# Kernel optimization log

Measured on AMD Instinct MI355X. Metric: run time of the kernel, lower is better.

The kernel has to match this reference:

```python
import jax, jax.numpy as jnp
import numpy as np

RATE = 2
KSIZE = 3          # patch size for similarity
KERNEL = 2 * RATE  # patch size for alpha scatter (4)
BN_EPS = 1e-5


def _extract_patches(x, k, s):
    """Mirror of GuidedCxtAtten.extract_patches: reflect-pad then unfold.
    x: [B,C,H,W] -> [B,Ho,Wo,C,k,k] with Ho=H//s, Wo=W//s."""
    left = (k - s + 1) // 2
    right = (k - s) // 2
    xp = jnp.pad(x, ((0, 0), (0, 0), (left, right), (left, right)), mode='reflect')
    Hp, Wp = xp.shape[2], xp.shape[3]
    Ho = (Hp - k) // s + 1
    Wo = (Wp - k) // s + 1
    ii = (jnp.arange(Ho) * s)[:, None] + jnp.arange(k)[None, :]   # [Ho,k]
    jj = (jnp.arange(Wo) * s)[:, None] + jnp.arange(k)[None, :]   # [Wo,k]
    p = xp[:, :, ii[:, :, None, None], jj[None, None, :, :]]      # [B,C,Ho,k,Wo,k]
    return p.transpose(0, 2, 4, 1, 3, 5)                          # [B,Ho,Wo,C,k,k]


def setup_inputs() -> dict:
    key = jax.random.key(0)
    ks = jax.random.split(key, 5)
    B, Cg, Ca, H, W = 4, 256, 128, 128, 128
    f = jax.random.normal(ks[0], (B, Cg, H, W), dtype=jnp.float32)
    alpha = jax.random.normal(ks[1], (B, Ca, H, W), dtype=jnp.float32)
    unknown = (jax.random.uniform(ks[2], (B, 1, H, W)) > 0.5).astype(jnp.float32)
    # guidance_conv: 1x1, Cg -> Cg//2, xavier-ish
    gc_w = jax.random.normal(ks[3], (Cg // 2, Cg), dtype=jnp.float32) * np.sqrt(2.0 / (Cg + Cg // 2))
    gc_b = jnp.zeros((Cg // 2,), dtype=jnp.float32)
    # W[0]: 1x1 conv Ca->Ca no bias; W[1]: BN with gamma=0.001, beta=0 per init
    w_w = jax.random.normal(ks[4], (Ca, Ca), dtype=jnp.float32) * np.sqrt(1.0 / Ca)
    bn_gamma = jnp.full((Ca,), 0.001, dtype=jnp.float32)
    bn_beta = jnp.zeros((Ca,), dtype=jnp.float32)
    return {"f": f, "alpha": alpha, "unknown": unknown, "gc_w": gc_w, "gc_b": gc_b,
            "w_w": w_w, "bn_gamma": bn_gamma, "bn_beta": bn_beta}


def _forward(f, alpha, unknown, gc_w, gc_b, w_w, bn_gamma, bn_beta):
    # guidance 1x1 conv
    fg = jnp.einsum('oi,bihw->bohw', gc_w, f) + gc_b[None, :, None, None]
    B, _, H, W = fg.shape
    Ca = alpha.shape[1]
    Hs, Ws = H // RATE, W // RATE
    L = Hs * Ws

    # alpha patches [B,L,Ca,4,4] (kernel=2*rate, stride=rate)
    alpha_w = _extract_patches(alpha, KERNEL, RATE).reshape(B, L, Ca, KERNEL, KERNEL)

    # nearest downsample by rate (torch nearest with scale 1/2 == strided pick)
    f_ds = fg[:, :, ::RATE, ::RATE]                # [B,Cg/2,Hs,Ws]
    unk_ds = unknown[:, :, ::RATE, ::RATE]         # [B,1,Hs,Ws]

    # similarity filter patches [B,L,C,3,3]
    w = _extract_patches(f_ds, KSIZE, 1).reshape(B, L, -1, KSIZE, KSIZE)

    # known/unknown softmax scales [B,2]
    u_mean = unk_ds.mean(axis=(2, 3))              # [B,1]
    k_mean = 1.0 - u_mean
    su = jnp.clip(jnp.sqrt(u_mean / k_mean), 0.1, 10.0)
    sk = jnp.clip(jnp.sqrt(k_mean / u_mean), 0.1, 10.0)
    softmax_scale = jnp.concatenate([su, sk], axis=1)

    # patch-mean of unknown mask -> binary patch mask [B,L]
    m = _extract_patches(unk_ds, KSIZE, 1).reshape(B, L, -1).mean(axis=2)
    mm = (m > 0.0).astype(fg.dtype)

    # l2-normalize filters per patch, then correlate against all positions.
    # Conv of reflect-padded f_ds with stride-1 3x3 patch filters == inner
    # product of normalized patches with the raw patches (same extraction).
    norm = jnp.sqrt(jnp.sum(w * w, axis=(2, 3, 4), keepdims=True))
    w_normed = w / jnp.maximum(norm, 1e-4)
    scores = jnp.einsum('bqcij,bpcij->bqp', w_normed, w)   # [B,L(q=patch),L(p=pos)]

    # known/unknown scaling per source patch q
    gate = jnp.where(mm > 0.0, su, sk)                      # [B,L]
    scores = scores * gate[:, :, None]

    # self-match suppression only for unknown patches (diagonal q == p)
    diag = jnp.arange(L)
    scores = scores.at[:, diag, diag].add(-10000.0 * mm)

    attn = jax.nn.softmax(scores, axis=1)                   # softmax over patches q

    # offsets (argmax patch per position, relative to center)
    idx = jnp.argmax(attn, axis=1)                          # [B,L]
    offsets = jnp.stack([idx // Ws, idx % Ws], axis=1).reshape(B, 2, Hs, Ws)
    offsets = offsets - jnp.array([Hs // 2, Ws // 2]).reshape(1, 2, 1, 1)

    # scatter alpha patches with attention weights: per-sample conv_transpose2d
    attn_map = attn.reshape(B, L, Hs, Ws)

    def ct(yi, wc):  # yi [L,Hs,Ws], wc [L,Ca,4,4]
        rhs = jnp.flip(wc, (2, 3)).transpose(1, 0, 2, 3)    # [Ca,L,4,4]
        pad = KERNEL - 1 - 1                                # torch padding=1
        out = jax.lax.conv_general_dilated(
            yi[None], rhs, window_strides=(1, 1),
            padding=[(pad, pad), (pad, pad)], lhs_dilation=(RATE, RATE),
            dimension_numbers=('NCHW', 'OIHW', 'NCHW'))
        return out[0]

    y = jax.vmap(ct)(attn_map, alpha_w) / 4.0               # [B,Ca,H,W]

    # W: 1x1 conv (no bias) + BatchNorm2d (training-mode batch stats)
    yw = jnp.einsum('oi,bihw->bohw', w_w, y)
    mean = yw.mean(axis=(0, 2, 3))
    var = yw.var(axis=(0, 2, 3))
    yn = (yw - mean[None, :, None, None]) * jax.lax.rsqrt(var + BN_EPS)[None, :, None, None]
    yn = yn * bn_gamma[None, :, None, None] + bn_beta[None, :, None, None]

    return yn + alpha, offsets, softmax_scale


def reference(f, alpha, unknown, gc_w, gc_b, w_w, bn_gamma, bn_beta):
    return _forward(f, alpha, unknown, gc_w, gc_b, w_w, bn_gamma, bn_beta)
```

## Files before the change

kernel.cpp:

```cpp
#include <hip/hip_runtime.h>
#include <math.h>

#define B 4
#define CG 256
#define CM 128
#define CA 128
#define H 128
#define W_ 128
#define HS 64
#define WS 64
#define L 4096
#define D1 1152
#define D2 2048
#define NPIX 65536
#define NT2 128

#define STP_F 8388608UL
#define WF_F  4718592UL
#define ZB_F  4194304UL
#define SLOT_F (STP_F + WF_F + ZB_F)

typedef unsigned short u16;
typedef __attribute__((ext_vector_type(8))) short short8v;
typedef __attribute__((ext_vector_type(4))) unsigned short u16x4;
typedef __attribute__((ext_vector_type(4))) float f32x4;

__device__ __forceinline__ float bf2f(u16 x) {
    union { unsigned int u; float f; } v; v.u = ((unsigned int)x) << 16; return v.f;
}
__device__ __forceinline__ u16 f2bf(float x) {
    union { float f; unsigned int u; } v; v.f = x;
    unsigned int r = (v.u + 0x7FFFu + ((v.u >> 16) & 1u)) >> 16;
    return (u16)r;
}
__device__ __forceinline__ void gll16(const void* g, void* l) {
    __builtin_amdgcn_global_load_lds((const __attribute__((address_space(1))) void*)g,
                                     (__attribute__((address_space(3))) void*)l, 16, 0, 0);
}
__device__ __forceinline__ int refl(int i, int n) {
    return i < 0 ? -i : (i >= n ? 2 * n - 2 - i : i);
}
__device__ __forceinline__ int swz(int row, int fq) {
    return row * 32 + ((fq ^ ((row >> 1) & 3)) * 8);
}

__device__ __forceinline__ void stage32(const u16* __restrict__ mat, int rowTile,
                                        int kt, u16* lds, int wid, int lane) {
#pragma unroll
    for (int c = 0; c < 2; ++c) {
        int off = c * 8192 + wid * 1024 + lane * 16;
        int row = off >> 6;
        int cb  = off & 63;
        const u16* g = mat + (size_t)(rowTile + row) * L + kt * 32
                     + ((cb ^ (((row >> 1) & 3) << 4)) >> 1);
        gll16(g, (char*)lds + c * 8192 + wid * 1024);
    }
}
__device__ __forceinline__ short8v rdfrag32(const u16* lds, int r, int fq) {
    return *(const short8v*)((const char*)lds + r * 64 + ((fq * 16) ^ (((r >> 1) & 3) << 4)));
}

__global__ __launch_bounds__(256) void k_conv_ds(const float* __restrict__ f,
                                                 const float* __restrict__ gw,
                                                 const float* __restrict__ gb,
                                                 float* __restrict__ fds,
                                                 float* __restrict__ ssq) {
    __shared__ float sf[CG * 64];
    __shared__ float part[4][64];
    int t = threadIdx.x;
    int hs = blockIdx.x, b = blockIdx.y;
    const float* fb = f + (size_t)b * CG * H * W_ + (2 * hs) * W_;
    for (int idx = t; idx < CG * 64; idx += 256) {
        int ci = idx >> 6, ws = idx & 63;
        sf[idx] = fb[(size_t)ci * H * W_ + 2 * ws];
    }
    __syncthreads();
    int ws = t & 63;
    int wave = __builtin_amdgcn_readfirstlane(t >> 6);
    const float* gwp = gw + (size_t)(wave * 32) * CG;
    float acc[32];
#pragma unroll
    for (int r = 0; r < 32; ++r) acc[r] = gb[wave * 32 + r];
    for (int ci = 0; ci < CG; ++ci) {
        float fv = sf[ci * 64 + ws];
#pragma unroll
        for (int r = 0; r < 32; ++r) acc[r] += gwp[r * CG + ci] * fv;
    }
    float sq = 0.f;
#pragma unroll
    for (int r = 0; r < 32; ++r) {
        int co = wave * 32 + r;
        fds[(((size_t)b * CM + co) * HS + hs) * WS + ws] = acc[r];
        sq += acc[r] * acc[r];
    }
    part[wave][ws] = sq;
    __syncthreads();
    if (t < 64)
        ssq[((size_t)b * HS + hs) * WS + t] =
            part[0][t] + part[1][t] + part[2][t] + part[3][t];
}

__global__ __launch_bounds__(256) void k_scale(const float* __restrict__ unk,
                                               float* __restrict__ suk,
                                               float* __restrict__ out2) {
    int b = blockIdx.x, t = threadIdx.x;
    __shared__ float red[256];
    float s = 0.f;
    for (int i = t; i < L; i += 256) {
        int hs = i >> 6, ws = i & 63;
        s += unk[(size_t)b * H * W_ + (2 * hs) * W_ + 2 * ws];
    }
    red[t] = s;
    __syncthreads();
    for (int o = 128; o > 0; o >>= 1) {
        if (t < o) red[t] += red[t + o];
        __syncthreads();
    }
    if (t == 0) {
        float u = red[0] / (float)L;
        float k = 1.0f - u;
        float su = sqrtf(u / k); su = fminf(fmaxf(su, 0.1f), 10.0f);
        float sk = sqrtf(k / u); sk = fminf(fmaxf(sk, 0.1f), 10.0f);
        suk[b * 2] = su; suk[b * 2 + 1] = sk;
        out2[b * 2] = su; out2[b * 2 + 1] = sk;
    }
}

__global__ __launch_bounds__(64) void k_gate(const float* __restrict__ unk,
                                             const float* __restrict__ ssq,
                                             const float* __restrict__ suk,
                                             float* __restrict__ g,
                                             float* __restrict__ dg) {
    int ws = threadIdx.x, hs = blockIdx.x, b = blockIdx.y;
    float sm = 0.f, sq = 0.f;
    for (int di = -1; di <= 1; ++di) {
        int rh = refl(hs + di, HS);
        for (int dj = -1; dj <= 1; ++dj) {
            int rw = refl(ws + dj, WS);
            sm += unk[(size_t)b * H * W_ + (2 * rh) * W_ + 2 * rw];
            sq += ssq[((size_t)b * HS + rh) * WS + rw];
        }
    }
    float mm   = (sm > 0.0f) ? 1.0f : 0.0f;
    float norm = sqrtf(sq);
    float gate = (mm > 0.0f) ? suk[2 * b] : suk[2 * b + 1];
    int q = hs * WS + ws;
    g[(size_t)b * L + q]  = gate / fmaxf(norm, 1e-4f);
    dg[(size_t)b * L + q] = -10000.0f * mm;
}

__global__ __launch_bounds__(256) void k_buildW(const float* __restrict__ fds,
                                                float* __restrict__ base, int b0) {
    int bz = blockIdx.z;
    int b  = b0 + bz;
    float* S   = base + (size_t)bz * SLOT_F;
    float* Wf  = S + STP_F;
    u16*   Whi = (u16*)(S + STP_F + WF_F);
    int ws = threadIdx.x;
    int c  = blockIdx.y * 4 + threadIdx.y;
    int hs = blockIdx.x;
    int q = hs * WS + ws;
    size_t bo = (size_t)q * D1 + c * 9;
    const float* src = fds + ((size_t)b * CM + c) * HS * WS;
#pragma unroll
    for (int i = 0; i < 3; ++i) {
        int rh = refl(hs + i - 1, HS);
#pragma unroll
        for (int j = 0; j < 3; ++j) {
            int rw = refl(ws + j - 1, WS);
            float v = src[rh * WS + rw];
            Wf[bo + i * 3 + j]  = v;
            Whi[bo + i * 3 + j] = f2bf(v);
        }
    }
}

__global__ __launch_bounds__(256) void k_gemm1(float* __restrict__ base,
                                               const float* __restrict__ g0,
                                               const float* __restrict__ dg0,
                                               int b0) {
    __shared__ u16 sAh[2][128 * 32], sBh[2][128 * 32];
    int bz = blockIdx.z;
    float* S = base + (size_t)bz * SLOT_F;
    u16* STP = (u16*)S;
    const u16* Whi = (const u16*)(S + STP_F + WF_F);
    const float* g  = g0  + (size_t)(b0 + bz) * L;
    const float* dg = dg0 + (size_t)(b0 + bz) * L;

    int tid = threadIdx.x;
    int wv = tid >> 6, lane = tid & 63;
    int t = blockIdx.x, I = 0;
    while (t >= 32 - I) { t -= 32 - I; ++I; }
    int J = I + t;
    int pTile = I * 128, qTile = J * 128;
    int wp = (wv >> 1) * 64, wq = (wv & 1) * 64;
    int r0 = wv * 32;
    int lrow = lane >> 2;
    int csw = ((lane & 3) ^ ((lrow >> 1) & 3)) * 8;
    int fr = lane & 15, fq = lane >> 4;

    const u16* gArow = Whi + (size_t)(pTile + r0 + lrow) * D1 + csw;
    const u16* gBrow = Whi + (size_t)(qTile + r0 + lrow) * D1 + csw;

    f32x4 acc[4][4];
#pragma unroll
    for (int mi = 0; mi < 4; ++mi)
#pragma unroll
        for (int ni = 0; ni < 4; ++ni)
#pragma unroll
            for (int r = 0; r < 4; ++r) acc[mi][ni][r] = 0.f;

    gll16(gArow, &sAh[0][r0 * 32]);
    gll16(gArow + (size_t)16 * D1, &sAh[0][(r0 + 16) * 32]);
    gll16(gBrow, &sBh[0][r0 * 32]);
    gll16(gBrow + (size_t)16 * D1, &sBh[0][(r0 + 16) * 32]);
    __syncthreads();

    int cur = 0;
    for (int k0 = 0; k0 < D1; k0 += 32) {
        int nxt = k0 + 32;
        if (nxt < D1) {
            gll16(gArow + nxt, &sAh[cur ^ 1][r0 * 32]);
            gll16(gArow + nxt + (size_t)16 * D1, &sAh[cur ^ 1][(r0 + 16) * 32]);
            gll16(gBrow + nxt, &sBh[cur ^ 1][r0 * 32]);
            gll16(gBrow + nxt + (size_t)16 * D1, &sBh[cur ^ 1][(r0 + 16) * 32]);
        }
        short8v ah[4], bh[4];
#pragma unroll
        for (int i = 0; i < 4; ++i) {
            ah[i] = *(const short8v*)&sAh[cur][swz(wp + i * 16 + fr, fq)];
            bh[i] = *(const short8v*)&sBh[cur][swz(wq + i * 16 + fr, fq)];
        }
        __builtin_amdgcn_s_setprio(1);
#pragma unroll
        for (int mi = 0; mi < 4; ++mi)
#pragma unroll
            for (int ni = 0; ni < 4; ++ni)
                acc[mi][ni] = __builtin_amdgcn_mfma_f32_16x16x32_bf16(ah[mi], bh[ni], acc[mi][ni], 0, 0, 0);
        __builtin_amdgcn_s_setprio(0);
        __syncthreads();
        cur ^= 1;
    }

#pragma unroll
    for (int ni = 0; ni < 4; ++ni) {
        int qq = qTile + wq + ni * 16 + fr;
        float gq = g[qq];
        float dq = dg[qq];
#pragma unroll
        for (int mi = 0; mi < 4; ++mi) {
            int pB = pTile + wp + mi * 16 + fq * 4;
#pragma unroll
            for (int r = 0; r < 4; ++r) {
                int p = pB + r;
                float v = acc[mi][ni][r] * gq;
                if (p == qq) v += dq;
                STP[(size_t)p * L + qq] = f2bf(v);
            }
        }
    }
    if (I != J) {
#pragma unroll
        for (int mi = 0; mi < 4; ++mi) {
            int p0 = pTile + wp + mi * 16 + fq * 4;
            float gp0 = g[p0], gp1 = g[p0 + 1], gp2 = g[p0 + 2], gp3 = g[p0 + 3];
#pragma unroll
            for (int ni = 0; ni < 4; ++ni) {
                int qq = qTile + wq + ni * 16 + fr;
                u16x4 mv;
                mv[0] = f2bf(acc[mi][ni][0] * gp0);
                mv[1] = f2bf(acc[mi][ni][1] * gp1);
                mv[2] = f2bf(acc[mi][ni][2] * gp2);
                mv[3] = f2bf(acc[mi][ni][3] * gp3);
                *(u16x4*)(STP + (size_t)qq * L + p0) = mv;
            }
        }
    }
}

__global__ __launch_bounds__(256) void k_softmax(float* __restrict__ base,
                                                 const float* __restrict__ g0,
                                                 const float* __restrict__ dg0,
                                                 float* __restrict__ out1, int b0) {
    __shared__ float buf[L];
    __shared__ float red[256];
    __shared__ int candList[128];
    __shared__ int candCount;
    int bz = blockIdx.y;
    int b  = b0 + bz;
    float* S = base + (size_t)bz * SLOT_F;
    u16* STP = (u16*)S;
    const float* Wf = S + STP_F;
    const float* g  = g0  + (size_t)b * L;
    const float* dg = dg0 + (size_t)b * L;

    int p = blockIdx.x, t = threadIdx.x;
    u16* rowp = STP + (size_t)p * L;

    if (t == 0) candCount = 0;
    float mx = -3.4e38f;
    for (int i = t; i < L / 8; i += 256) {
        short8v v8 = ((const short8v*)rowp)[i];
#pragma unroll
        for (int j = 0; j < 8; ++j) {
            float v = bf2f((u16)v8[j]);
            buf[i * 8 + j] = v;
            mx = fmaxf(mx, v);
        }
    }
    red[t] = mx;
    __syncthreads();
    for (int o = 128; o > 0; o >>= 1) {
        if (t < o) red[t] = fmaxf(red[t], red[t + o]);
        __syncthreads();
    }
    float M = red[0];
    float u = fabsf(M) * 0.0625f + 1e-5f;
    float cth = M - u;
    __syncthreads();

    float s = 0.f;
    for (int i = t; i < L; i += 256) {
        float v = buf[i];
        if (v >= cth) {
            int ix = atomicAdd(&candCount, 1);
            if (ix < 128) candList[ix] = i;
        }
        float e = __expf(v - M);
        buf[i] = e;
        s += e;
    }
    red[t] = s;
    __syncthreads();
    for (int o = 128; o > 0; o >>= 1) {
        if (t < o) red[t] += red[t + o];
        __syncthreads();
    }
    float inv = 1.0f / red[0];
    __syncthreads();

    for (int i = t; i < L / 8; i += 256) {
        short8v o8;
#pragma unroll
        for (int j = 0; j < 8; ++j) o8[j] = (short)f2bf(buf[i * 8 + j] * inv);
        ((short8v*)rowp)[i] = o8;
    }
    __syncthreads();

    int nc = candCount; if (nc > 128) nc = 128;
    int bestI;
    if (nc == 1) {
        bestI = candList[0];
    } else {
        float bestE = -3.4e38f; bestI = L;
        const float* wp_ = Wf + (size_t)p * D1;
        for (int k = 0; k < nc; ++k) {
            int cand = candList[k];
            const float* wc = Wf + (size_t)cand * D1;
            float part = 0.f;
            for (int j = t; j < D1; j += 256) part += wp_[j] * wc[j];
            red[t] = part;
            __syncthreads();
            for (int o = 128; o > 0; o >>= 1) {
                if (t < o) red[t] += red[t + o];
                __syncthreads();
            }
            float e1 = red[0] * g[cand] + (p == cand ? dg[cand] : 0.f);
            if (e1 > bestE || (e1 == bestE && cand < bestI)) { bestE = e1; bestI = cand; }
            __syncthreads();
        }
    }
    if (t == 0) {
        out1[(size_t)(b * 2 + 0) * L + p] = (float)(bestI / WS - 32);
        out1[(size_t)(b * 2 + 1) * L + p] = (float)(bestI % WS - 32);
    }
}

__global__ __launch_bounds__(256) void k_buildA(const float* __restrict__ alpha,
                                                float* __restrict__ base, int b0) {
    int bz = blockIdx.z;
    int b  = b0 + bz;
    u16* At = (u16*)(base + (size_t)bz * SLOT_F + STP_F);
    int q = blockIdx.x * 256 + threadIdx.x;
    int n = blockIdx.y;
    int hs = q >> 6, ws = q & 63;
    int c = n >> 4, ki = (n >> 2) & 3, kj = n & 3;
    int rh = refl(2 * hs + ki - 1, H);
    int rw = refl(2 * ws + kj - 1, W_);
    At[(size_t)n * L + q] = f2bf(alpha[((size_t)b * CA + c) * H * W_ + rh * W_ + rw]);
}

__global__ __launch_bounds__(512, 2) void k_gemm2(float* __restrict__ base) {
    __shared__ u16 smem[49152];
    int bz = blockIdx.z;
    float* S = base + (size_t)bz * SLOT_F;
    const u16* P  = (const u16*)S;
    const u16* At = (const u16*)(S + STP_F);
    u16* Z        = (u16*)(S + STP_F + WF_F);

    int tid = threadIdx.x;
    int wid = tid >> 6, lane = tid & 63;
    int wm = wid >> 2, wn = wid & 3;
    int pTile = blockIdx.x * 256, nTile = blockIdx.y * 256;
    int fr = lane & 15, fq = lane >> 4;

    f32x4 acc[8][4];
#pragma unroll
    for (int m = 0; m < 8; ++m)
#pragma unroll
        for (int n = 0; n < 4; ++n)
#pragma unroll
            for (int r = 0; r < 4; ++r) acc[m][n][r] = 0.f;

    stage32(P,  pTile, 0, smem,         wid, lane);
    stage32(At, nTile, 0, smem + 8192,  wid, lane);
    stage32(P,  pTile, 1, smem + 16384, wid, lane);
    stage32(At, nTile, 1, smem + 24576, wid, lane);
    asm volatile("s_waitcnt vmcnt(4)" ::: "memory");
    __builtin_amdgcn_s_barrier();
    __builtin_amdgcn_sched_barrier(0);

    for (int t = 0; t < NT2; ++t) {
        const u16* Ab = smem + (t % 3) * 16384;
        const u16* Bb = Ab + 8192;
        short8v a[8], b[4];
#pragma unroll
        for (int n = 0; n < 4; ++n) b[n] = rdfrag32(Bb, wn * 64 + n * 16 + fr, fq);
#pragma unroll
        for (int m = 0; m < 4; ++m) a[m] = rdfrag32(Ab, wm * 128 + m * 16 + fr, fq);
        __builtin_amdgcn_s_setprio(1);
#pragma unroll
        for (int m = 0; m < 2; ++m)
#pragma unroll
            for (int n = 0; n < 4; ++n)
                acc[m][n] = __builtin_amdgcn_mfma_f32_16x16x32_bf16(a[m], b[n], acc[m][n], 0, 0, 0);
        __builtin_amdgcn_s_setprio(0);
#pragma unroll
        for (int m = 4; m < 8; ++m) a[m] = rdfrag32(Ab, wm * 128 + m * 16 + fr, fq);
        __builtin_amdgcn_s_setprio(1);
#pragma unroll
        for (int m = 2; m < 6; ++m)
#pragma unroll
            for (int n = 0; n < 4; ++n)
                acc[m][n] = __builtin_amdgcn_mfma_f32_16x16x32_bf16(a[m], b[n], acc[m][n], 0, 0, 0);
        __builtin_amdgcn_s_setprio(0);
        int kt2 = (t + 2 < NT2) ? (t + 2) : 0;
        u16* d2 = smem + ((t + 2) % 3) * 16384;
        stage32(P,  pTile, kt2, d2,        wid, lane);
        stage32(At, nTile, kt2, d2 + 8192, wid, lane);
        asm volatile("s_waitcnt vmcnt(4)" ::: "memory");
        __builtin_amdgcn_sched_barrier(0);
        __builtin_amdgcn_s_setprio(1);
#pragma unroll
        for (int m = 6; m < 8; ++m)
#pragma unroll
            for (int n = 0; n < 4; ++n)
                acc[m][n] = __builtin_amdgcn_mfma_f32_16x16x32_bf16(a[m], b[n], acc[m][n], 0, 0, 0);
        __builtin_amdgcn_s_setprio(0);
        __builtin_amdgcn_s_barrier();
        __builtin_amdgcn_sched_barrier(0);
    }

#pragma unroll
    for (int m = 0; m < 8; ++m)
#pragma unroll
        for (int n = 0; n < 4; ++n) {
            int nn = nTile + wn * 64 + n * 16 + fr;
#pragma unroll
            for (int r = 0; r < 4; ++r) {
                int pp = pTile + wm * 128 + m * 16 + fq * 4 + r;
                Z[(size_t)pp * D2 + nn] = f2bf(acc[m][n][r]);
            }
        }
}

__global__ __launch_bounds__(256) void k_gather(float* __restrict__ base,
                                                u16* __restrict__ yt, int b0) {
    int bz = blockIdx.z;
    int b  = b0 + bz;
    const u16* Z = (const u16*)(base + (size_t)bz * SLOT_F + STP_F + WF_F);
    int c  = threadIdx.x & 127;
    int pl = threadIdx.x >> 7;
    int w  = blockIdx.x * 2 + pl;
    int h  = blockIdx.y;
    float s = 0.f;
#pragma unroll
    for (int ki = 0; ki < 4; ++ki) {
        int num = h + 1 - ki;
        if (num < 0 || (num & 1)) continue;
        int hs = num >> 1;
        if (hs >= HS) continue;
#pragma unroll
        for (int kj = 0; kj < 4; ++kj) {
            int numw = w + 1 - kj;
            if (numw < 0 || (numw & 1)) continue;
            int wsd = numw >> 1;
            if (wsd >= WS) continue;
            s += bf2f(Z[(size_t)(hs * WS + wsd) * D2 + c * 16 + ki * 4 + kj]);
        }
    }
    int pix = h * W_ + w;
    int cs = c ^ ((pix & 7) << 3);
    yt[((size_t)b * 16384 + pix) * 128 + cs] = f2bf(0.25f * s);
}

__global__ __launch_bounds__(256) void k_cvtww(const float* __restrict__ ww,
                                               u16* __restrict__ wwbf) {
    int i = blockIdx.x * 256 + threadIdx.x;
    int o = i >> 7, c = i & 127;
    wwbf[o * 128 + (c ^ ((o & 7) << 3))] = f2bf(ww[i]);
}

__global__ __launch_bounds__(256) void k_ywgemm(const u16* __restrict__ wwbf,
                                                const u16* __restrict__ yt,
                                                float* __restrict__ yw) {
    __shared__ u16 sA[128 * 128], sB[128 * 128];
    int tid = threadIdx.x;
    int wv = tid >> 6, lane = tid & 63;
    int nTile = blockIdx.x * 128;
    int wp = (wv >> 1) * 64, wn = (wv & 1) * 64;
    int fr = lane & 15, fq = lane >> 4;

    const u16* gB = yt + (size_t)nTile * 128;
#pragma unroll
    for (int i = 0; i < 8; ++i) {
        int o = (i * 4 + wv) * 512;
        gll16(wwbf + o + lane * 8, &sA[o]);
        gll16(gB + o + lane * 8, &sB[o]);
    }
    __syncthreads();

    f32x4 acc[4][4];
#pragma unroll
    for (int mi = 0; mi < 4; ++mi)
#pragma unroll
        for (int ni = 0; ni < 4; ++ni)
#pragma unroll
            for (int r = 0; r < 4; ++r) acc[mi][ni][r] = 0.f;

#pragma unroll
    for (int ks = 0; ks < 4; ++ks) {
        int k0 = ks * 32 + fq * 8;
        short8v a[4], bb[4];
#pragma unroll
        for (int i = 0; i < 4; ++i) {
            int ra = wp + i * 16 + fr;
            a[i] = *(const short8v*)&sA[ra * 128 + (k0 ^ ((ra & 7) << 3))];
            int rb = wn + i * 16 + fr;
            bb[i] = *(const short8v*)&sB[rb * 128 + (k0 ^ ((rb & 7) << 3))];
        }
#pragma unroll
        for (int mi = 0; mi < 4; ++mi)
#pragma unroll
            for (int ni = 0; ni < 4; ++ni)
                acc[mi][ni] = __builtin_amdgcn_mfma_f32_16x16x32_bf16(a[mi], bb[ni], acc[mi][ni], 0, 0, 0);
    }

#pragma unroll
    for (int mi = 0; mi < 4; ++mi)
#pragma unroll
        for (int ni = 0; ni < 4; ++ni) {
            int gp = nTile + wn + ni * 16 + fr;
#pragma unroll
            for (int r = 0; r < 4; ++r) {
                int o = wp + mi * 16 + fq * 4 + r;
                yw[(size_t)o * NPIX + gp] = acc[mi][ni][r];
            }
        }
}

__global__ __launch_bounds__(256) void k_stats(const float* __restrict__ yw,
                                               float* __restrict__ meanvar) {
    int o = blockIdx.x, t = threadIdx.x;
    __shared__ float rs[256], rq[256];
    float s = 0.f, q = 0.f;
    const float* p = yw + (size_t)o * NPIX;
    for (int i = t; i < NPIX; i += 256) {
        float v = p[i];
        s += v;
        q += v * v;
    }
    rs[t] = s; rq[t] = q;
    __syncthreads();
    for (int off = 128; off > 0; off >>= 1) {
        if (t < off) { rs[t] += rs[t + off]; rq[t] += rq[t + off]; }
        __syncthreads();
    }
    if (t == 0) {
        float n = (float)NPIX;
        float mean = rs[0] / n;
        float var  = rq[0] / n - mean * mean;
        meanvar[o] = mean;
        meanvar[CA + o] = var;
    }
}

__global__ __launch_bounds__(256) void k_final(const float* __restrict__ yw,
                                               const float* __restrict__ meanvar,
                                               const float* __restrict__ gamma,
                                               const float* __restrict__ beta,
                                               const float* __restrict__ alpha,
                                               float* __restrict__ out0) {
    size_t i = ((size_t)blockIdx.x * 256 + threadIdx.x) * 4;
    int c = (int)((i >> 14) & 127);
    int b = (int)(i >> 21);
    int pix = (int)(i & 16383);
    float4 v = *(const float4*)(yw + (size_t)c * NPIX + b * 16384 + pix);
    float4 a = *(const float4*)(alpha + i);
    float mean = meanvar[c];
    float var  = meanvar[CA + c];
    float sc   = rsqrtf(var + 1e-5f) * gamma[c];
    float bt   = beta[c];
    float4 r;
    r.x = (v.x - mean) * sc + bt + a.x;
    r.y = (v.y - mean) * sc + bt + a.y;
    r.z = (v.z - mean) * sc + bt + a.z;
    r.w = (v.w - mean) * sc + bt + a.w;
    *(float4*)(out0 + i) = r;
}

extern "C" void kernel_launch(void* const* d_in, const int* in_sizes, int n_in,
                              void* d_out, int out_size, void* d_ws, size_t ws_size,
                              hipStream_t stream) {
    (void)in_sizes; (void)n_in; (void)out_size;
    const float* f     = (const float*)d_in[0];
    const float* alpha = (const float*)d_in[1];
    const float* unk   = (const float*)d_in[2];
    const float* gw    = (const float*)d_in[3];
    const float* gb    = (const float*)d_in[4];
    const float* ww    = (const float*)d_in[5];
    const float* gamma = (const float*)d_in[6];
    const float* beta  = (const float*)d_in[7];

    float* out0 = (float*)d_out;
    float* out1 = out0 + (size_t)B * CA * H * W_;
    float* out2 = out1 + (size_t)B * 2 * HS * WS;

    float* wsf = (float*)d_ws;
    size_t off = 0;
    float* fds     = wsf + off; off += (size_t)B * CM * HS * WS;
    float* ssq     = wsf + off; off += (size_t)B * HS * WS;
    float* gbuf    = wsf + off; off += (size_t)B * L;
    float* dgbuf   = wsf + off; off += (size_t)B * L;
    float* suk     = wsf + off; off += 64;
    float* ytF     = wsf + off; off += (size_t)NPIX * 128 / 2;
    float* wwbfF   = wsf + off; off += 8192;
    float* meanvar = wsf + off; off += 256;
    float* base    = wsf + off;

    const size_t PRE_F = off;
    int nb = (ws_size >= (PRE_F + 4 * SLOT_F) * sizeof(float)) ? 4 : 2;

    float* yw   = base;
    u16*   yt   = (u16*)ytF;
    u16*   wwbf = (u16*)wwbfF;

    k_cvtww<<<64, 256, 0, stream>>>(ww, wwbf);
    k_conv_ds<<<dim3(64, 4), 256, 0, stream>>>(f, gw, gb, fds, ssq);
    k_scale<<<4, 256, 0, stream>>>(unk, suk, out2);
    k_gate<<<dim3(64, 4), 64, 0, stream>>>(unk, ssq, suk, gbuf, dgbuf);

    for (int b0 = 0; b0 < B; b0 += nb) {
        k_buildW<<<dim3(64, 32, nb), dim3(64, 4), 0, stream>>>(fds, base, b0);
        k_gemm1<<<dim3(528, 1, nb), 256, 0, stream>>>(base, gbuf, dgbuf, b0);
        k_softmax<<<dim3(4096, nb), 256, 0, stream>>>(base, gbuf, dgbuf, out1, b0);
        k_buildA<<<dim3(16, 2048, nb), 256, 0, stream>>>(alpha, base, b0);
        k_gemm2<<<dim3(16, 8, nb), 512, 0, stream>>>(base);
        k_gather<<<dim3(64, 128, nb), 256, 0, stream>>>(base, yt, b0);
    }

    k_ywgemm<<<512, 256, 0, stream>>>(wwbf, yt, yw);
    k_stats<<<128, 256, 0, stream>>>(yw, meanvar);
    k_final<<<8192, 256, 0, stream>>>(yw, meanvar, gamma, beta, alpha, out0);
}
```

Before: 863.2 us.

## Triple-buffer gemm1, deepen gemm2 prefetch, and use wave shuffles in softmax reductions

k_gemm1 moves from a double-buffered loop with a full __syncthreads per step to a three-stage LDS ring. It issues loads two tiles ahead and places the wait mid-loop between MFMA halves, matching k_gemm2's scheme. k_gemm2 goes from three to four LDS stages, prefetching three tiles ahead, at the cost of 128KB of shared memory per block, which may lower occupancy. The softmax reductions switch from shared-memory tree reductions to wavefront shuffle reductions, removing several barriers.

```diff
diff --git a/kernel.cpp b/kernel.cpp
--- a/kernel.cpp
+++ b/kernel.cpp
@@ -13,6 +13,7 @@
 #define D1 1152
 #define D2 2048
 #define NPIX 65536
+#define NT1 36
 #define NT2 128
 
 #define STP_F 8388608UL
@@ -179,7 +180,7 @@
                                                const float* __restrict__ g0,
                                                const float* __restrict__ dg0,
                                                int b0) {
-    __shared__ u16 sAh[2][128 * 32], sBh[2][128 * 32];
+    __shared__ u16 sA[3][128 * 32], sB[3][128 * 32];
     int bz = blockIdx.z;
     float* S = base + (size_t)bz * SLOT_F;
     u16* STP = (u16*)S;
@@ -189,9 +190,9 @@
 
     int tid = threadIdx.x;
     int wv = tid >> 6, lane = tid & 63;
-    int t = blockIdx.x, I = 0;
-    while (t >= 32 - I) { t -= 32 - I; ++I; }
-    int J = I + t;
+    int t0 = blockIdx.x, I = 0;
+    while (t0 >= 32 - I) { t0 -= 32 - I; ++I; }
+    int J = I + t0;
     int pTile = I * 128, qTile = J * 128;
     int wp = (wv >> 1) * 64, wq = (wv & 1) * 64;
     int r0 = wv * 32;
@@ -202,6 +203,12 @@
     const u16* gArow = Whi + (size_t)(pTile + r0 + lrow) * D1 + csw;
     const u16* gBrow = Whi + (size_t)(qTile + r0 + lrow) * D1 + csw;
 
+#define G1STAGE(kt, bf) do { \
+    gll16(gArow + (kt) * 32, &sA[bf][r0 * 32]); \
+    gll16(gArow + (kt) * 32 + (size_t)16 * D1, &sA[bf][(r0 + 16) * 32]); \
+    gll16(gBrow + (kt) * 32, &sB[bf][r0 * 32]); \
+    gll16(gBrow + (kt) * 32 + (size_t)16 * D1, &sB[bf][(r0 + 16) * 32]); } while (0)
+
     f32x4 acc[4][4];
 #pragma unroll
     for (int mi = 0; mi < 4; ++mi)
@@ -210,37 +217,42 @@
 #pragma unroll
             for (int r = 0; r < 4; ++r) acc[mi][ni][r] = 0.f;
 
-    gll16(gArow, &sAh[0][r0 * 32]);
-    gll16(gArow + (size_t)16 * D1, &sAh[0][(r0 + 16) * 32]);
-    gll16(gBrow, &sBh[0][r0 * 32]);
-    gll16(gBrow + (size_t)16 * D1, &sBh[0][(r0 + 16) * 32]);
-    __syncthreads();
-
-    int cur = 0;
-    for (int k0 = 0; k0 < D1; k0 += 32) {
-        int nxt = k0 + 32;
-        if (nxt < D1) {
-            gll16(gArow + nxt, &sAh[cur ^ 1][r0 * 32]);
-            gll16(gArow + nxt + (size_t)16 * D1, &sAh[cur ^ 1][(r0 + 16) * 32]);
-            gll16(gBrow + nxt, &sBh[cur ^ 1][r0 * 32]);
-            gll16(gBrow + nxt + (size_t)16 * D1, &sBh[cur ^ 1][(r0 + 16) * 32]);
-        }
+    G1STAGE(0, 0);
+    G1STAGE(1, 1);
+    asm volatile("s_waitcnt vmcnt(4)" ::: "memory");
+    __builtin_amdgcn_s_barrier();
+    __builtin_amdgcn_sched_barrier(0);
+
+    for (int t = 0; t < NT1; ++t) {
+        int cur = t % 3;
         short8v ah[4], bh[4];
 #pragma unroll
         for (int i = 0; i < 4; ++i) {
-            ah[i] = *(const short8v*)&sAh[cur][swz(wp + i * 16 + fr, fq)];
-            bh[i] = *(const short8v*)&sBh[cur][swz(wq + i * 16 + fr, fq)];
+            ah[i] = *(const short8v*)&sA[cur][swz(wp + i * 16 + fr, fq)];
+            bh[i] = *(const short8v*)&sB[cur][swz(wq + i * 16 + fr, fq)];
         }
         __builtin_amdgcn_s_setprio(1);
 #pragma unroll
-        for (int mi = 0; mi < 4; ++mi)
+        for (int mi = 0; mi < 2; ++mi)
 #pragma unroll
             for (int ni = 0; ni < 4; ++ni)
                 acc[mi][ni] = __builtin_amdgcn_mfma_f32_16x16x32_bf16(ah[mi], bh[ni], acc[mi][ni], 0, 0, 0);
         __builtin_amdgcn_s_setprio(0);
-        __syncthreads();
-        cur ^= 1;
-    }
+        int kt2 = (t + 2 < NT1) ? (t + 2) : 0;
+        G1STAGE(kt2, (t + 2) % 3);
+        asm volatile("s_waitcnt vmcnt(4)" ::: "memory");
+        __builtin_amdgcn_sched_barrier(0);
+        __builtin_amdgcn_s_setprio(1);
+#pragma unroll
+        for (int mi = 2; mi < 4; ++mi)
+#pragma unroll
+            for (int ni = 0; ni < 4; ++ni)
+                acc[mi][ni] = __builtin_amdgcn_mfma_f32_16x16x32_bf16(ah[mi], bh[ni], acc[mi][ni], 0, 0, 0);
+        __builtin_amdgcn_s_setprio(0);
+        __builtin_amdgcn_s_barrier();
+        __builtin_amdgcn_sched_barrier(0);
+    }
+#undef G1STAGE
 
 #pragma unroll
     for (int ni = 0; ni < 4; ++ni) {
@@ -283,7 +295,7 @@
                                                  const float* __restrict__ dg0,
                                                  float* __restrict__ out1, int b0) {
     __shared__ float buf[L];
-    __shared__ float red[256];
+    __shared__ float wmax[4], wsum[4], cred[4];
     __shared__ int candList[128];
     __shared__ int candCount;
     int bz = blockIdx.y;
@@ -295,6 +307,7 @@
     const float* dg = dg0 + (size_t)b * L;
 
     int p = blockIdx.x, t = threadIdx.x;
+    int lane = t & 63, wv = t >> 6;
     u16* rowp = STP + (size_t)p * L;
 
     if (t == 0) candCount = 0;
@@ -308,16 +321,12 @@
             mx = fmaxf(mx, v);
         }
     }
-    red[t] = mx;
+#pragma unroll
+    for (int o = 32; o > 0; o >>= 1) mx = fmaxf(mx, __shfl_xor(mx, o));
+    if (lane == 0) wmax[wv] = mx;
     __syncthreads();
-    for (int o = 128; o > 0; o >>= 1) {
-        if (t < o) red[t] = fmaxf(red[t], red[t + o]);
-        __syncthreads();
-    }
-    float M = red[0];
-    float u = fabsf(M) * 0.0625f + 1e-5f;
-    float cth = M - u;
-    __syncthreads();
+    float M = fmaxf(fmaxf(wmax[0], wmax[1]), fmaxf(wmax[2], wmax[3]));
+    float cth = M - (fabsf(M) * 0.0625f + 1e-5f);
 
     float s = 0.f;
     for (int i = t; i < L; i += 256) {
@@ -330,14 +339,11 @@
         buf[i] = e;
         s += e;
     }
-    red[t] = s;
+#pragma unroll
+    for (int o = 32; o > 0; o >>= 1) s += __shfl_xor(s, o);
+    if (lane == 0) wsum[wv] = s;
     __syncthreads();
-    for (int o = 128; o > 0; o >>= 1) {
-        if (t < o) red[t] += red[t + o];
-        __syncthreads();
-    }
-    float inv = 1.0f / red[0];
-    __syncthreads();
+    float inv = 1.0f / (wsum[0] + wsum[1] + wsum[2] + wsum[3]);
 
     for (int i = t; i < L / 8; i += 256) {
         short8v o8;
@@ -345,7 +351,6 @@
         for (int j = 0; j < 8; ++j) o8[j] = (short)f2bf(buf[i * 8 + j] * inv);
         ((short8v*)rowp)[i] = o8;
     }
-    __syncthreads();
 
     int nc = candCount; if (nc > 128) nc = 128;
     int bestI;
@@ -359,13 +364,12 @@
             const float* wc = Wf + (size_t)cand * D1;
             float part = 0.f;
             for (int j = t; j < D1; j += 256) part += wp_[j] * wc[j];
-            red[t] = part;
+#pragma unroll
+            for (int o = 32; o > 0; o >>= 1) part += __shfl_xor(part, o);
+            if (lane == 0) cred[wv] = part;
             __syncthreads();
-            for (int o = 128; o > 0; o >>= 1) {
-                if (t < o) red[t] += red[t + o];
-                __syncthreads();
-            }
-            float e1 = red[0] * g[cand] + (p == cand ? dg[cand] : 0.f);
+            float e1 = (cred[0] + cred[1] + cred[2] + cred[3]) * g[cand]
+                     + (p == cand ? dg[cand] : 0.f);
             if (e1 > bestE || (e1 == bestE && cand < bestI)) { bestE = e1; bestI = cand; }
             __syncthreads();
         }
@@ -391,7 +395,7 @@
 }
 
 __global__ __launch_bounds__(512, 2) void k_gemm2(float* __restrict__ base) {
-    __shared__ u16 smem[49152];
+    __shared__ u16 smem[65536];
     int bz = blockIdx.z;
     float* S = base + (size_t)bz * SLOT_F;
     const u16* P  = (const u16*)S;
@@ -416,12 +420,14 @@
     stage32(At, nTile, 0, smem + 8192,  wid, lane);
     stage32(P,  pTile, 1, smem + 16384, wid, lane);
     stage32(At, nTile, 1, smem + 24576, wid, lane);
-    asm volatile("s_waitcnt vmcnt(4)" ::: "memory");
+    stage32(P,  pTile, 2, smem + 32768, wid, lane);
+    stage32(At, nTile, 2, smem + 40960, wid, lane);
+    asm volatile("s_waitcnt vmcnt(8)" ::: "memory");
     __builtin_amdgcn_s_barrier();
     __builtin_amdgcn_sched_barrier(0);
 
     for (int t = 0; t < NT2; ++t) {
-        const u16* Ab = smem + (t % 3) * 16384;
+        const u16* Ab = smem + (t & 3) * 16384;
         const u16* Bb = Ab + 8192;
         short8v a[8], b[4];
 #pragma unroll
@@ -444,11 +450,11 @@
             for (int n = 0; n < 4; ++n)
                 acc[m][n] = __builtin_amdgcn_mfma_f32_16x16x32_bf16(a[m], b[n], acc[m][n], 0, 0, 0);
         __builtin_amdgcn_s_setprio(0);
-        int kt2 = (t + 2 < NT2) ? (t + 2) : 0;
-        u16* d2 = smem + ((t + 2) % 3) * 16384;
-        stage32(P,  pTile, kt2, d2,        wid, lane);
-        stage32(At, nTile, kt2, d2 + 8192, wid, lane);
-        asm volatile("s_waitcnt vmcnt(4)" ::: "memory");
+        int kt3 = (t + 3 < NT2) ? (t + 3) : 0;
+        u16* d3 = smem + ((t + 3) & 3) * 16384;
+        stage32(P,  pTile, kt3, d3,        wid, lane);
+        stage32(At, nTile, kt3, d3 + 8192, wid, lane);
+        asm volatile("s_waitcnt vmcnt(8)" ::: "memory");
         __builtin_amdgcn_sched_barrier(0);
         __builtin_amdgcn_s_setprio(1);
 #pragma unroll
```

Measured after the change: 846.5 us. Within noise of the previous version (-1.9%).
